# Kernel tuning notes

Hardware: AMD Instinct MI355X
Metric: run time of the kernel (lower is better)

## Reference

```python
import jax, jax.numpy as jnp
import numpy as np


def _nearest(t, H, W):
    # torch F.interpolate(mode='nearest'): idx = floor(out_i * in/out)
    Hin, Win = t.shape[1], t.shape[2]
    ri = jnp.floor(jnp.arange(H) * (Hin / H)).astype(jnp.int32)
    ci = jnp.floor(jnp.arange(W) * (Win / W)).astype(jnp.int32)
    return t[:, ri][:, :, ci]


def setup_inputs() -> dict:
    key = jax.random.key(0)
    k1, k2, k3, k4 = jax.random.split(key, 4)
    N, A, H, W, C = 4, 256, 256, 256, 19
    features = jax.random.normal(k1, (N, A, H, W), dtype=jnp.float32)
    fc_weight = jax.random.normal(k2, (C, A, 1, 1), dtype=jnp.float32) * 0.05
    y = jax.random.normal(k3, (N, C, H, W), dtype=jnp.float32)
    t = jax.random.randint(k4, (N, 2 * H, 2 * W), 0, 20)
    target_x = jnp.where(t == 19, 255, t).astype(jnp.int32)  # some ignore pixels
    Ave = jnp.zeros((C + 1, A), dtype=jnp.float32)
    CoVariance = jnp.zeros((C + 1, A), dtype=jnp.float32)
    Amount = jnp.zeros((C + 1,), dtype=jnp.float32)
    ratio = jnp.ones((1,), dtype=jnp.float32)
    return {"features": features, "fc_weight": fc_weight, "y": y, "Ave": Ave,
            "CoVariance": CoVariance, "Amount": Amount, "ratio": ratio,
            "target_x": target_x}


def reference(features, fc_weight, y, Ave, CoVariance, Amount, ratio, target_x):
    N, A, H, W = features.shape
    C = fc_weight.shape[0]          # 19 real classes
    Cn = C + 1                      # estimator has an extra ignore slot
    tgt = _nearest(target_x, H, W).reshape(-1)                 # [NHW]
    feat = features.transpose(0, 2, 3, 1).reshape(-1, A)       # [NHW, A]
    y_flat = y.transpose(0, 2, 3, 1).reshape(-1, C)            # [NHW, C]

    # ---- EstimatorCV.update_CV (features detached in original) ----
    f_d = jax.lax.stop_gradient(feat)
    lab_u = jnp.where(tgt == 255, C, tgt)                      # 255 -> class 19
    counts = jax.ops.segment_sum(jnp.ones_like(f_d[:, 0]), lab_u, num_segments=Cn)
    denom = jnp.maximum(counts, 1.0)[:, None]
    ave = jax.ops.segment_sum(f_d, lab_u, num_segments=Cn) / denom        # [Cn,A]
    var = jax.ops.segment_sum((f_d - ave[lab_u]) ** 2, lab_u, num_segments=Cn) / denom
    w = counts / (counts + Amount)
    w = jnp.where(jnp.isnan(w), 0.0, w)[:, None]               # nan (0/0) -> 0
    add_cv = w * (1.0 - w) * (Ave - ave) ** 2
    CoV = CoVariance * (1.0 - w) + var * w + add_cv            # [Cn,A] (detached)
    CoV = jax.lax.stop_gradient(CoV)

    # ---- isda_aug: sigma2[n,c] = ratio * sum_a (W[c]-W[k_n])^2 * CV[k_n] ----
    lab_a = jnp.where(tgt == 255, 0, tgt)
    valid = (tgt != 255).astype(feat.dtype)
    Wm = fc_weight.reshape(C, A)
    Wk = Wm[lab_a]                                             # [NHW, A]
    CVk = CoV[lab_a]                                           # [NHW, A]
    t1 = jnp.einsum('ca,na->nc', Wm * Wm, CVk)
    t2 = jnp.einsum('ca,na->nc', Wm, Wk * CVk)
    t3 = jnp.sum(Wk * Wk * CVk, axis=1, keepdims=True)
    sigma2 = ratio[0] * (t1 - 2.0 * t2 + t3)                   # [NHW, C]
    aug = y_flat + 0.5 * sigma2 * valid[:, None]
    return aug.reshape(N, H, W, C).transpose(0, 3, 1, 2)
```

## Files before the change

### kernel.cpp

```cpp
#include <hip/hip_runtime.h>
#include <hip/hip_bf16.h>
#include <stdint.h>

#define N_IMG 4
#define A_DIM 256
#define HW    65536
#define C_CLS 19
#define NPIX  (N_IMG*HW)
#define CHUNK 512
#define NCHUNK (NPIX/CHUNK)
#define TSPLIT 16

#define OFF_LAB  0
#define OFF_S    262144
#define OFF_HIST 263680
#define OFF_P2   304640
#define OFF_P1   927232
#define P1_ROW_BYTES (C_CLS*2*A_DIM*4)

__device__ __forceinline__ void load_group(float4 (&buf)[8], const float4* f4, int g) {
#pragma unroll
    for (int q = 0; q < 8; ++q) buf[q] = f4[g * 8 + q];
}

__device__ __forceinline__ void proc_group(const float4 (&buf)[8], int g,
                                           const unsigned* lw,
                                           float2* __restrict__ b0,
                                           float2* __restrict__ b1, int t) {
#pragma unroll
    for (int q = 0; q < 8; ++q) {
        unsigned w = lw[g * 8 + q];
        const float4 vv = buf[q];
#pragma unroll
        for (int i = 0; i < 4; ++i) {
            int lb = (w >> (8 * i)) & 255;
            float v = (i == 0) ? vv.x : (i == 1) ? vv.y : (i == 2) ? vv.z : vv.w;
            bool ok = lb < C_CLS;
            float vm = ok ? v : 0.0f;
            int row = ok ? lb : 0;
            int idx = (row << 8) + t;
            if (i & 1) {
                float2 x = b1[idx];
                x.x += vm; x.y = fmaf(vm, vm, x.y);
                b1[idx] = x;
            } else {
                float2 x = b0[idx];
                x.x += vm; x.y = fmaf(vm, vm, x.y);
                b0[idx] = x;
            }
        }
    }
}

__global__ __launch_bounds__(256) void kB_stats(const float* __restrict__ features,
                                                const int* __restrict__ tgt,
                                                uint8_t* __restrict__ lab,
                                                float2* __restrict__ partial,
                                                int* __restrict__ hists, int nblk) {
    __shared__ float2 bins0[C_CLS * A_DIM];
    __shared__ float2 bins1[C_CLS * A_DIM];
    __shared__ unsigned labw[CHUNK / 4];
    __shared__ int hist[20];
    int t = threadIdx.x;
    for (int i = t; i < C_CLS * A_DIM; i += 256) {
        bins0[i] = make_float2(0.f, 0.f);
        bins1[i] = make_float2(0.f, 0.f);
    }
    if (t < 20) hist[t] = 0;

    for (int chk = blockIdx.x; chk < NCHUNK; chk += nblk) {
        int n = chk >> 7;
        int p0 = (chk & 127) * CHUNK;
        __syncthreads();

        const float4* f4 = (const float4*)(features + (((size_t)(n * A_DIM + t)) << 16) + p0);
        float4 bufA[8], bufB[8];
        load_group(bufA, f4, 0);
        load_group(bufB, f4, 1);

        if (t < CHUNK / 4) {
            int p = p0 + t * 4;
            int h = p >> 8, w = p & 255;
            const int* row = tgt + (n << 18) + (h << 10) + (w << 1);
            int4 u0 = *(const int4*)(row);
            int4 u1 = *(const int4*)(row + 4);
            int l0 = (u0.x == 255) ? 19 : u0.x;
            int l1 = (u0.z == 255) ? 19 : u0.z;
            int l2 = (u1.x == 255) ? 19 : u1.x;
            int l3 = (u1.z == 255) ? 19 : u1.z;
            unsigned packed = (unsigned)l0 | ((unsigned)l1 << 8)
                            | ((unsigned)l2 << 16) | ((unsigned)l3 << 24);
            labw[t] = packed;
            ((unsigned*)(lab + n * HW + p0))[t] = packed;
            atomicAdd(&hist[l0], 1); atomicAdd(&hist[l1], 1);
            atomicAdd(&hist[l2], 1); atomicAdd(&hist[l3], 1);
        }
        __syncthreads();

#pragma unroll 1
        for (int g = 0; g < 16; g += 2) {
            proc_group(bufA, g, labw, bins0, bins1, t);
            if (g + 2 < 16) load_group(bufA, f4, g + 2);
            proc_group(bufB, g + 1, labw, bins0, bins1, t);
            if (g + 3 < 16) load_group(bufB, f4, g + 3);
        }
    }
    __syncthreads();
    float2* dst = partial + (size_t)blockIdx.x * (C_CLS * A_DIM);
    for (int i = t; i < C_CLS * A_DIM; i += 256)
        dst[i] = make_float2(bins0[i].x + bins1[i].x, bins0[i].y + bins1[i].y);
    if (t < 20) hists[blockIdx.x * 20 + t] = hist[t];
}

__global__ __launch_bounds__(256) void kC1a(const float2* __restrict__ partial,
                                            float2* __restrict__ p2, int nblk) {
    int c = blockIdx.x;
    int s = blockIdx.y;
    int a = threadIdx.x;
    int per = nblk / TSPLIT;
    float sum = 0.f, sq = 0.f;
    for (int b = s * per; b < (s + 1) * per; ++b) {
        float2 v = partial[(size_t)b * (C_CLS * A_DIM) + c * A_DIM + a];
        sum += v.x; sq += v.y;
    }
    p2[(s * C_CLS + c) * A_DIM + a] = make_float2(sum, sq);
}

__global__ __launch_bounds__(256) void kCF(const float2* __restrict__ p2,
                                           const int* __restrict__ hists, int nblk,
                                           const float* __restrict__ Amount,
                                           const float* __restrict__ Ave,
                                           const float* __restrict__ CoVin,
                                           const float* __restrict__ W,
                                           const float* __restrict__ ratio,
                                           float* __restrict__ S) {
    int k = blockIdx.x, t = threadIdx.x;
    if (k == 19) {
        if (t < C_CLS) S[19 * C_CLS + t] = 0.0f;
        return;
    }
    __shared__ float sred[4];
    __shared__ float red[C_CLS][4];
    int lane = t & 63, wv = t >> 6;
    int csum = 0;
    for (int b = t; b < nblk; b += 256) csum += hists[b * 20 + k];
#pragma unroll
    for (int o = 32; o > 0; o >>= 1) csum += __shfl_xor(csum, o, 64);
    if (lane == 0) sred[wv] = (float)csum;
    __syncthreads();
    float cnt = sred[0] + sred[1] + sred[2] + sred[3];

    float sum = 0.f, sq = 0.f;
#pragma unroll
    for (int s = 0; s < TSPLIT; ++s) {
        float2 v = p2[(s * C_CLS + k) * A_DIM + t];
        sum += v.x; sq += v.y;
    }
    float denom = fmaxf(cnt, 1.0f);
    float ave = sum / denom;
    float var = (sq - 2.0f * ave * sum + ave * ave * cnt) / denom;
    float dw = cnt + Amount[k];
    float w = (dw != 0.0f) ? (cnt / dw) : 0.0f;
    float d = Ave[k * A_DIM + t] - ave;
    float cv = CoVin[k * A_DIM + t] * (1.0f - w) + var * w + w * (1.0f - w) * d * d;

    float wk = W[k * A_DIM + t];
    for (int c = 0; c < C_CLS; ++c) {
        float dd = W[c * A_DIM + t] - wk;
        float term = dd * dd * cv;
#pragma unroll
        for (int o = 32; o > 0; o >>= 1) term += __shfl_xor(term, o, 64);
        if (lane == 0) red[c][wv] = term;
    }
    __syncthreads();
    if (t < C_CLS)
        S[k * C_CLS + t] = 0.5f * ratio[0] * (red[t][0] + red[t][1] + red[t][2] + red[t][3]);
}

__global__ __launch_bounds__(256) void kD_apply(const float* __restrict__ y,
                                                const uint8_t* __restrict__ lab,
                                                const float* __restrict__ S,
                                                float* __restrict__ out) {
    __shared__ float sS[20 * C_CLS];
    int t = threadIdx.x;
    for (int i = t; i < 20 * C_CLS; i += 256) sS[i] = S[i];
    __syncthreads();
    int idx4 = blockIdx.x * 256 + t;
    int plane = idx4 >> 14;
    int p4 = idx4 & 16383;
    int n = plane / C_CLS;
    int c = plane - n * C_CLS;
    float4 yv = ((const float4*)y)[idx4];
    unsigned lw = *(((const unsigned*)(lab + n * HW)) + p4);
    float4 o;
    o.x = yv.x + sS[((lw      ) & 255) * C_CLS + c];
    o.y = yv.y + sS[((lw >> 8 ) & 255) * C_CLS + c];
    o.z = yv.z + sS[((lw >> 16) & 255) * C_CLS + c];
    o.w = yv.w + sS[((lw >> 24)      ) * C_CLS + c];
    ((float4*)out)[idx4] = o;
}

extern "C" void kernel_launch(void* const* d_in, const int* in_sizes, int n_in,
                              void* d_out, int out_size, void* d_ws, size_t ws_size,
                              hipStream_t stream) {
    const float* features  = (const float*)d_in[0];
    const float* fc_weight = (const float*)d_in[1];
    const float* y         = (const float*)d_in[2];
    const float* Ave       = (const float*)d_in[3];
    const float* CoVin     = (const float*)d_in[4];
    const float* Amount    = (const float*)d_in[5];
    const float* ratio     = (const float*)d_in[6];
    const int*   target_x  = (const int*)d_in[7];
    float* out             = (float*)d_out;

    char* ws = (char*)d_ws;
    uint8_t* lab    = (uint8_t*)(ws + OFF_LAB);
    float*   S      = (float*)(ws + OFF_S);
    int*     hists  = (int*)(ws + OFF_HIST);
    float2*  p2     = (float2*)(ws + OFF_P2);
    float2*  partial= (float2*)(ws + OFF_P1);

    size_t avail = (ws_size > (size_t)OFF_P1) ? (ws_size - OFF_P1) : 0;
    int nblk = (int)(avail / P1_ROW_BYTES);
    if (nblk > 512) nblk = 512;
    nblk &= ~15;
    if (nblk < 16) nblk = 16;

    kB_stats<<<nblk, 256, 0, stream>>>(features, target_x, lab, partial, hists, nblk);
    kC1a<<<dim3(C_CLS, TSPLIT), 256, 0, stream>>>(partial, p2, nblk);
    kCF<<<20, 256, 0, stream>>>(p2, hists, nblk, Amount, Ave, CoVin, fc_weight, ratio, S);
    kD_apply<<<(NPIX * C_CLS / 4) / 256, 256, 0, stream>>>(y, lab, S, out);
}
```

Baseline: 92.55 us.

## Remap stats kernel threads to channel pairs with float4 LDS bins; nontemporal output stores

```diff
diff --git a/kernel.cpp b/kernel.cpp
--- a/kernel.cpp
+++ b/kernel.cpp
@@ -18,37 +18,34 @@
 #define OFF_P1   927232
 #define P1_ROW_BYTES (C_CLS*2*A_DIM*4)
 
-__device__ __forceinline__ void load_group(float4 (&buf)[8], const float4* f4, int g) {
-#pragma unroll
-    for (int q = 0; q < 8; ++q) buf[q] = f4[g * 8 + q];
-}
-
-__device__ __forceinline__ void proc_group(const float4 (&buf)[8], int g,
-                                           const unsigned* lw,
-                                           float2* __restrict__ b0,
-                                           float2* __restrict__ b1, int t) {
-#pragma unroll
-    for (int q = 0; q < 8; ++q) {
-        unsigned w = lw[g * 8 + q];
-        const float4 vv = buf[q];
-#pragma unroll
-        for (int i = 0; i < 4; ++i) {
-            int lb = (w >> (8 * i)) & 255;
-            float v = (i == 0) ? vv.x : (i == 1) ? vv.y : (i == 2) ? vv.z : vv.w;
-            bool ok = lb < C_CLS;
-            float vm = ok ? v : 0.0f;
-            int row = ok ? lb : 0;
-            int idx = (row << 8) + t;
-            if (i & 1) {
-                float2 x = b1[idx];
-                x.x += vm; x.y = fmaf(vm, vm, x.y);
-                b1[idx] = x;
-            } else {
-                float2 x = b0[idx];
-                x.x += vm; x.y = fmaf(vm, vm, x.y);
-                b0[idx] = x;
-            }
-        }
+typedef float natf4 __attribute__((ext_vector_type(4)));
+
+
+__device__ __forceinline__ void load_pair(float4 (&X)[4], float4 (&Y)[4],
+                                          const float4* fe4, const float4* fo4, int g) {
+#pragma unroll
+    for (int k = 0; k < 4; ++k) {
+        X[k] = fe4[g * 4 + k];
+        Y[k] = fo4[g * 4 + k];
+    }
+}
+
+__device__ __forceinline__ void acc4pair(float4 X, float4 Y, unsigned w,
+                                         float4* __restrict__ bins, int c2) {
+#pragma unroll
+    for (int i = 0; i < 4; ++i) {
+        int lb = (w >> (8 * i)) & 255;
+        float vx = (i == 0) ? X.x : (i == 1) ? X.y : (i == 2) ? X.z : X.w;
+        float vy = (i == 0) ? Y.x : (i == 1) ? Y.y : (i == 2) ? Y.z : Y.w;
+        bool ok = lb < C_CLS;
+        float v0 = ok ? vx : 0.0f;
+        float v1 = ok ? vy : 0.0f;
+        int row = ok ? lb : 0;
+        int idx = (row << 7) + c2;
+        float4 x = bins[idx];
+        x.x += v0; x.y = fmaf(v0, v0, x.y);
+        x.z += v1; x.w = fmaf(v1, v1, x.w);
+        bins[idx] = x;
     }
 }
 
@@ -57,14 +54,17 @@
                                                 uint8_t* __restrict__ lab,
                                                 float2* __restrict__ partial,
                                                 int* __restrict__ hists, int nblk) {
-    __shared__ float2 bins0[C_CLS * A_DIM];
-    __shared__ float2 bins1[C_CLS * A_DIM];
+    __shared__ float4 binsA[C_CLS * 128];
+    __shared__ float4 binsB[C_CLS * 128];
     __shared__ unsigned labw[CHUNK / 4];
     __shared__ int hist[20];
     int t = threadIdx.x;
-    for (int i = t; i < C_CLS * A_DIM; i += 256) {
-        bins0[i] = make_float2(0.f, 0.f);
-        bins1[i] = make_float2(0.f, 0.f);
+    int hf = t >> 7;
+    int c2 = t & 127;
+    float4* bins = hf ? binsB : binsA;
+    for (int i = t; i < C_CLS * 128; i += 256) {
+        binsA[i] = make_float4(0.f, 0.f, 0.f, 0.f);
+        binsB[i] = make_float4(0.f, 0.f, 0.f, 0.f);
     }
     if (t < 20) hist[t] = 0;
 
@@ -73,10 +73,13 @@
         int p0 = (chk & 127) * CHUNK;
         __syncthreads();
 
-        const float4* f4 = (const float4*)(features + (((size_t)(n * A_DIM + t)) << 16) + p0);
-        float4 bufA[8], bufB[8];
-        load_group(bufA, f4, 0);
-        load_group(bufB, f4, 1);
+        const float* fe = features + (((size_t)(n * A_DIM + 2 * c2)) << 16)
+                        + p0 + (hf << 8);
+        const float4* fe4 = (const float4*)fe;
+        const float4* fo4 = fe4 + (HW / 4);
+        float4 XA[4], YA[4], XB[4], YB[4];
+        load_pair(XA, YA, fe4, fo4, 0);
+        load_pair(XB, YB, fe4, fo4, 1);
 
         if (t < CHUNK / 4) {
             int p = p0 + t * 4;
@@ -99,16 +102,24 @@
 
 #pragma unroll 1
         for (int g = 0; g < 16; g += 2) {
-            proc_group(bufA, g, labw, bins0, bins1, t);
-            if (g + 2 < 16) load_group(bufA, f4, g + 2);
-            proc_group(bufB, g + 1, labw, bins0, bins1, t);
-            if (g + 3 < 16) load_group(bufB, f4, g + 3);
+#pragma unroll
+            for (int k = 0; k < 4; ++k)
+                acc4pair(XA[k], YA[k], labw[(hf << 6) + (g << 2) + k], bins, c2);
+            if (g + 2 < 16) load_pair(XA, YA, fe4, fo4, g + 2);
+#pragma unroll
+            for (int k = 0; k < 4; ++k)
+                acc4pair(XB[k], YB[k], labw[(hf << 6) + ((g + 1) << 2) + k], bins, c2);
+            if (g + 3 < 16) load_pair(XB, YB, fe4, fo4, g + 3);
         }
     }
     __syncthreads();
     float2* dst = partial + (size_t)blockIdx.x * (C_CLS * A_DIM);
-    for (int i = t; i < C_CLS * A_DIM; i += 256)
-        dst[i] = make_float2(bins0[i].x + bins1[i].x, bins0[i].y + bins1[i].y);
+    for (int i = t; i < C_CLS * 128; i += 256) {
+        int row = i >> 7, cc = i & 127;
+        float4 a = binsA[i], b = binsB[i];
+        dst[row * A_DIM + 2 * cc]     = make_float2(a.x + b.x, a.y + b.y);
+        dst[row * A_DIM + 2 * cc + 1] = make_float2(a.z + b.z, a.w + b.w);
+    }
     if (t < 20) hists[blockIdx.x * 20 + t] = hist[t];
 }
 
@@ -192,12 +203,12 @@
     int c = plane - n * C_CLS;
     float4 yv = ((const float4*)y)[idx4];
     unsigned lw = *(((const unsigned*)(lab + n * HW)) + p4);
-    float4 o;
+    natf4 o;
     o.x = yv.x + sS[((lw      ) & 255) * C_CLS + c];
     o.y = yv.y + sS[((lw >> 8 ) & 255) * C_CLS + c];
     o.z = yv.z + sS[((lw >> 16) & 255) * C_CLS + c];
     o.w = yv.w + sS[((lw >> 24)      ) * C_CLS + c];
-    ((float4*)out)[idx4] = o;
+    __builtin_nontemporal_store(o, (natf4*)out + idx4);
 }
 
 extern "C" void kernel_launch(void* const* d_in, const int* in_sizes, int n_in,
```

Measured after the change: 109.9 us. +18.8%, slower.
